# Performance work log

Measured on AMD Instinct MI355X. Metric: run time of the kernel, lower is better.

## Reference

```python
import jax, jax.numpy as jnp
import numpy as np

DIM = 2560
N_HEAD = 32
HEAD_DIM = 80
ROT_DIM = 32  # head_dim * partial_rotary_factor
INTER = 10240
EPS = 1e-5
BASE = 10000.0


def setup_inputs() -> dict:
    key = jax.random.key(0)
    ks = jax.random.split(key, 12)
    B, S, D, I = 1, 2048, DIM, INTER
    s = lambda k, shape, scale: (jax.random.normal(k, shape, jnp.float32) * scale)
    return {
        "x": s(ks[0], (B, S, D), 1.0),
        "input_pos": jnp.arange(S, dtype=jnp.int32),
        "mask": jnp.tril(jnp.ones((S, S), dtype=bool)),
        "ln_w": jnp.ones((D,), jnp.float32),
        "ln_b": jnp.zeros((D,), jnp.float32),
        "wqkv_w": s(ks[1], (3 * D, D), 0.02),
        "wqkv_b": jnp.zeros((3 * D,), jnp.float32),
        "wo_w": s(ks[2], (D, D), 0.02),
        "wo_b": jnp.zeros((D,), jnp.float32),
        "w1_w": s(ks[3], (I, D), 0.02),
        "w1_b": jnp.zeros((I,), jnp.float32),
        "w2_w": s(ks[4], (D, I), 0.02),
        "w2_b": jnp.zeros((D,), jnp.float32),
    }


def _rope_cos_sin(positions):
    # positions: [S] int; returns cos,sin of shape [S, ROT_DIM]
    inv_freq = 1.0 / (BASE ** (jnp.arange(0, ROT_DIM, 2, dtype=jnp.float32) / ROT_DIM))
    freqs = positions.astype(jnp.float32)[:, None] * inv_freq[None, :]  # [S, ROT/2]
    emb = jnp.concatenate([freqs, freqs], axis=-1)  # [S, ROT]
    return jnp.cos(emb), jnp.sin(emb)


def _rotate_half(t):
    t1, t2 = jnp.split(t, 2, axis=-1)
    return jnp.concatenate([-t2, t1], axis=-1)


def _apply_rope(t, cos, sin):
    # t: [B,H,S,hd]; rotary applied to first ROT_DIM dims (partial rotary)
    t_rot, t_pass = t[..., :ROT_DIM], t[..., ROT_DIM:]
    t_rot = t_rot * cos[None, None] + _rotate_half(t_rot) * sin[None, None]
    return jnp.concatenate([t_rot, t_pass], axis=-1)


def reference(x, input_pos, mask, ln_w, ln_b, wqkv_w, wqkv_b, wo_w, wo_b,
              w1_w, w1_b, w2_w, w2_b):
    B, S, D = x.shape
    H, hd = N_HEAD, HEAD_DIM
    # shared LayerNorm (parallel block)
    mu = jnp.mean(x, axis=-1, keepdims=True)
    var = jnp.mean(jnp.square(x - mu), axis=-1, keepdims=True)
    h = (x - mu) * jax.lax.rsqrt(var + EPS) * ln_w + ln_b

    # fused QKV
    qkv = h @ wqkv_w.T + wqkv_b  # [B,S,3D]
    q, k, v = jnp.split(qkv, 3, axis=-1)
    q = q.reshape(B, S, H, hd).transpose(0, 2, 1, 3)  # [B,H,S,hd]
    k = k.reshape(B, S, H, hd).transpose(0, 2, 1, 3)
    v = v.reshape(B, S, H, hd).transpose(0, 2, 1, 3)

    cos, sin = _rope_cos_sin(input_pos)
    q = _apply_rope(q, cos, sin)
    k = _apply_rope(k, cos, sin)

    # causal attention
    scores = jnp.einsum("bhqd,bhkd->bhqk", q, k) / np.sqrt(hd).astype(np.float32)
    scores = jnp.where(mask[None, None], scores, jnp.float32(-1e9))
    attn = jax.nn.softmax(scores, axis=-1)
    y = jnp.einsum("bhqk,bhkd->bhqd", attn, v)  # [B,H,S,hd]
    y = y.transpose(0, 2, 1, 3).reshape(B, S, D)
    attn_out = y @ wo_w.T + wo_b

    # fused MLP (phi2: gelu_new / tanh approx)
    ffn = jax.nn.gelu(h @ w1_w.T + w1_b, approximate=True) @ w2_w.T + w2_b

    return attn_out + ffn + x
```

## Files before the change

kernel.cpp:

```cpp
#include <hip/hip_runtime.h>
#include <cstdint>

#define S_LEN 2048
#define DMODEL 2560
#define NHEADS 32
#define HDIM 80
#define DINTER 10240

typedef unsigned short u16;
typedef __bf16 bf16x8 __attribute__((ext_vector_type(8)));
typedef float f32x4 __attribute__((ext_vector_type(4)));

__device__ __forceinline__ float us2f(u16 u) {
  return __builtin_bit_cast(float, ((uint32_t)u) << 16);
}
__device__ __forceinline__ u16 f2us(float f) {
  uint32_t x = __builtin_bit_cast(uint32_t, f);
  x += 0x7fffu + ((x >> 16) & 1u);
  return (u16)(x >> 16);
}

typedef __attribute__((address_space(1))) void gas_void;
typedef __attribute__((address_space(3))) void las_void;
__device__ __forceinline__ void gld16(const void* g, void* l) {
  __builtin_amdgcn_global_load_lds((gas_void*)g, (las_void*)l, 16, 0, 0);
}

#define VMW(N) asm volatile("s_waitcnt vmcnt(" #N ")" ::: "memory")
#define BARRIER()                          \
  do {                                     \
    asm volatile("" ::: "memory");         \
    __builtin_amdgcn_s_barrier();          \
    asm volatile("" ::: "memory");         \
  } while (0)

__global__ void f2b_kernel(const float* __restrict__ src, u16* __restrict__ dst) {
  const size_t i = ((size_t)blockIdx.x * 256 + threadIdx.x) * 8;
  const float4 a = *(const float4*)(src + i);
  const float4 b = *(const float4*)(src + i + 4);
  u16 o[8] = {f2us(a.x), f2us(a.y), f2us(a.z), f2us(a.w),
              f2us(b.x), f2us(b.y), f2us(b.z), f2us(b.w)};
  *(uint4*)(dst + i) = *(uint4*)o;
}

__global__ void initout_kernel(const float* __restrict__ x,
                               const float* __restrict__ wo_b,
                               const float* __restrict__ w2_b,
                               float* __restrict__ out) {
  const size_t idx = ((size_t)blockIdx.x * 256 + threadIdx.x) * 4;
  const int c0 = (int)(idx % DMODEL);
  const float4 vx = *(const float4*)(x + idx);
  const float4 b1 = *(const float4*)(wo_b + c0);
  const float4 b2 = *(const float4*)(w2_b + c0);
  float4 vo;
  vo.x = vx.x + b1.x + b2.x;
  vo.y = vx.y + b1.y + b2.y;
  vo.z = vx.z + b1.z + b2.z;
  vo.w = vx.w + b1.w + b2.w;
  *(float4*)(out + idx) = vo;
}

__global__ void ln_kernel(const float* __restrict__ x, const float* __restrict__ w,
                          const float* __restrict__ b, u16* __restrict__ h) {
  const int s = blockIdx.x, tid = threadIdx.x;
  const float* xr = x + (size_t)s * DMODEL;
  float v[10];
  float sum = 0.f, sq = 0.f;
#pragma unroll
  for (int j = 0; j < 10; j++) {
    v[j] = xr[tid + j * 256];
    sum += v[j];
    sq += v[j] * v[j];
  }
#pragma unroll
  for (int o = 32; o > 0; o >>= 1) {
    sum += __shfl_down(sum, o, 64);
    sq += __shfl_down(sq, o, 64);
  }
  __shared__ float red[8];
  const int wave = tid >> 6, lane = tid & 63;
  if (lane == 0) { red[wave] = sum; red[4 + wave] = sq; }
  __syncthreads();
  sum = red[0] + red[1] + red[2] + red[3];
  sq = red[4] + red[5] + red[6] + red[7];
  const float mu = sum * (1.0f / DMODEL);
  const float var = sq * (1.0f / DMODEL) - mu * mu;
  const float rstd = rsqrtf(var + 1e-5f);
  u16* hr = h + (size_t)s * DMODEL;
#pragma unroll
  for (int j = 0; j < 10; j++) {
    const int d = tid + j * 256;
    hr[d] = f2us((v[j] - mu) * rstd * w[d] + b[d]);
  }
}

template <int ACT, int MODE>
__launch_bounds__(512, 2)
__global__ void gemm256(const u16* __restrict__ A, const u16* __restrict__ B,
                        const float* __restrict__ bias, void* __restrict__ Cv,
                        int M, int N, int K) {
  __shared__ __align__(16) u16 lds[4][16384];
  const int tid = threadIdx.x;
  const int w = tid >> 6, lane = tid & 63;
  const int quad = lane >> 4, l15 = lane & 15;
  const int wm = w >> 2, wn = w & 3;

  const int nwg = gridDim.x * gridDim.y;
  const int flat = blockIdx.x + gridDim.x * blockIdx.y;
  const int swz = (flat & 7) * (nwg >> 3) + (flat >> 3);
  const int ntN = N >> 8;
  const int bm = swz / ntN, bn = swz % ntN;

  const int Kc = K / gridDim.z;
  const int k0 = Kc * blockIdx.z;
  const int nt = Kc >> 6;

  const int stgCol = (((lane & 7) ^ ((lane >> 3) & 7)) * 8);
  const u16* Ag = A + ((size_t)bm * 256 + w * 8 + (lane >> 3)) * K + k0 + stgCol;
  const u16* Bg = B + ((size_t)bn * 256 + w * 8 + (lane >> 3)) * K + k0 + stgCol;

  const int q8 = quad * 8;
  const int swz3 = (l15 & 7) * 8;
  const int arow = wm * 64 + l15;
  const int brow = wn * 32 + l15;

#define STG_HALF(MAT, GP, BUF, HF, KT)                                       \
  do {                                                                       \
    gld16((GP) + (size_t)((HF) * 128) * K + (size_t)(KT) * 64,               \
          &lds[(BUF) * 2 + (MAT)][(HF) * 8192 + w * 512]);                   \
    gld16((GP) + (size_t)((HF) * 128 + 64) * K + (size_t)(KT) * 64,          \
          &lds[(BUF) * 2 + (MAT)][(HF) * 8192 + 4096 + w * 512]);            \
  } while (0)

#define LDS_A(DST, BUF, MH)                                                  \
  _Pragma("unroll") for (int mf_ = 0; mf_ < 4; mf_++)                        \
  _Pragma("unroll") for (int kk_ = 0; kk_ < 2; kk_++)                        \
      DST[mf_][kk_] = *(const bf16x8*)&lds[(BUF) * 2]                        \
          [(arow + (MH) * 128 + mf_ * 16) * 64 + ((kk_ * 32 + q8) ^ swz3)];

#define LDS_B(DST, BUF, NH)                                                  \
  _Pragma("unroll") for (int nf_ = 0; nf_ < 2; nf_++)                        \
  _Pragma("unroll") for (int kk_ = 0; kk_ < 2; kk_++)                        \
      DST[nf_][kk_] = *(const bf16x8*)&lds[(BUF) * 2 + 1]                    \
          [(brow + (NH) * 128 + nf_ * 16) * 64 + ((kk_ * 32 + q8) ^ swz3)];

#define MFMA_C(MH, NH, AF, BF)                                               \
  do {                                                                       \
    __builtin_amdgcn_s_setprio(1);                                           \
    _Pragma("unroll") for (int kk_ = 0; kk_ < 2; kk_++)                      \
    _Pragma("unroll") for (int mf_ = 0; mf_ < 4; mf_++)                      \
    _Pragma("unroll") for (int nf_ = 0; nf_ < 2; nf_++)                      \
        acc[(MH) * 4 + mf_][(NH) * 2 + nf_] =                                \
            __builtin_amdgcn_mfma_f32_16x16x32_bf16(                         \
                AF[mf_][kk_], BF[nf_][kk_],                                  \
                acc[(MH) * 4 + mf_][(NH) * 2 + nf_], 0, 0, 0);               \
    __builtin_amdgcn_s_setprio(0);                                           \
  } while (0)

  f32x4 acc[8][4] = {};
  bf16x8 aH0[4][2], aH1[4][2], bH0[2][2], bH1[2][2];

  STG_HALF(0, Ag, 0, 0, 0);
  STG_HALF(1, Bg, 0, 0, 0);
  STG_HALF(1, Bg, 0, 1, 0);
  STG_HALF(0, Ag, 0, 1, 0);
  VMW(4);
  BARRIER();
  LDS_A(aH0, 0, 0);
  LDS_B(bH0, 0, 0);

  for (int t = 0; t < nt; ++t) {
    const int bc = t & 1, ob = bc ^ 1;
    const bool more = (t + 1 < nt);
    VMW(0);
    BARRIER();
    if (more) {
      STG_HALF(0, Ag, ob, 0, t + 1);
      STG_HALF(1, Bg, ob, 0, t + 1);
    }
    LDS_B(bH1, bc, 1);
    MFMA_C(0, 0, aH0, bH0);
    if (more) STG_HALF(1, Bg, ob, 1, t + 1);
    LDS_A(aH1, bc, 1);
    MFMA_C(0, 1, aH0, bH1);
    if (more) STG_HALF(0, Ag, ob, 1, t + 1);
    MFMA_C(1, 1, aH1, bH1);
    VMW(4);
    BARRIER();
    MFMA_C(1, 0, aH1, bH0);
    if (more) {
      LDS_A(aH0, ob, 0);
      LDS_B(bH0, ob, 0);
    }
  }

#pragma unroll
  for (int nh = 0; nh < 2; nh++)
#pragma unroll
    for (int nf = 0; nf < 2; nf++) {
      const int col = bn * 256 + nh * 128 + wn * 32 + nf * 16 + l15;
      const float bv = (MODE == 0) ? bias[col] : 0.f;
#pragma unroll
      for (int mh = 0; mh < 2; mh++)
#pragma unroll
        for (int mf = 0; mf < 4; mf++) {
          const int row0 = bm * 256 + mh * 128 + wm * 64 + mf * 16 + quad * 4;
#pragma unroll
          for (int r = 0; r < 4; r++) {
            float v = acc[mh * 4 + mf][nh * 2 + nf][r] + bv;
            if (ACT == 1) {
              const float tt = v * (0.7978845608f + 0.0356774081f * v * v);
              v = 0.5f * v * (1.0f + tanhf(tt));
            }
            if (MODE == 0)
              ((u16*)Cv)[(size_t)(row0 + r) * N + col] = f2us(v);
            else
              atomicAdd((float*)Cv + (size_t)(row0 + r) * N + col, v);
          }
        }
    }
#undef STG_HALF
#undef LDS_A
#undef LDS_B
#undef MFMA_C
}

__global__ void rope_kernel(u16* __restrict__ qkv, const int* __restrict__ pos) {
  const int idx = blockIdx.x * 256 + threadIdx.x;
  const int i = idx & 15;
  const int which = (idx >> 4) & 1;
  const int hh = (idx >> 5) & 31;
  const int s = idx >> 10;
  const float p = (float)pos[s];
  const float freq = p * expf(-0.57564627324851f * (float)i);
  float sn, c;
  sincosf(freq, &sn, &c);
  u16* base = qkv + (size_t)s * (3 * DMODEL) + which * DMODEL + hh * HDIM + i;
  const float t0 = us2f(base[0]), t1 = us2f(base[16]);
  base[0] = f2us(t0 * c - t1 * sn);
  base[16] = f2us(t1 * c + t0 * sn);
}

__global__ void attn_kernel(const u16* __restrict__ qkv, u16* __restrict__ y) {
  const int qt = (int)gridDim.x - 1 - (int)blockIdx.x;
  const int h = blockIdx.y;
  const int tid = threadIdx.x, wave = tid >> 6, lane = tid & 63;
  const int quad = lane >> 4, l15 = lane & 15;
  const int qbase = qt * 64;

  __shared__ __align__(16) u16 Qs[64 * 104];
  __shared__ __align__(16) u16 Ks[2][64 * 104];
  __shared__ __align__(16) u16 Vts[2][80 * 88];
  __shared__ __align__(16) u16 Ps[4][2][16 * 40];

  if (tid < 128) {
    const int b = tid >> 6, r = tid & 63;
    u16* z = &Ks[b][r * 104 + 80];
    *(uint4*)z = uint4{0, 0, 0, 0};
    *(uint4*)(z + 8) = uint4{0, 0, 0, 0};
  } else if (tid < 192) {
    const int r = tid & 63;
    u16* z = &Qs[r * 104 + 80];
    *(uint4*)z = uint4{0, 0, 0, 0};
    *(uint4*)(z + 8) = uint4{0, 0, 0, 0};
    *(uint4*)(z + 16) = uint4{0, 0, 0, 0};
  }

  {
    const int r = tid >> 2, c = tid & 3;
    const u16* src = qkv + (size_t)(qbase + r) * (3 * DMODEL) + h * HDIM + c * 20;
    u16* dst = Qs + r * 104 + c * 20;
#pragma unroll
    for (int j = 0; j < 5; j++) {
      ushort4 uv = *(const ushort4*)(src + j * 4);
      ushort4 ov;
      ov.x = f2us(us2f(uv.x) * 0.11180339887f);
      ov.y = f2us(us2f(uv.y) * 0.11180339887f);
      ov.z = f2us(us2f(uv.z) * 0.11180339887f);
      ov.w = f2us(us2f(uv.w) * 0.11180339887f);
      *(ushort4*)(dst + j * 4) = ov;
    }
  }

  {
    const int r = tid >> 2, c4 = (tid & 3) * 20;
    const u16* sK = qkv + (size_t)r * (3 * DMODEL) + DMODEL + h * HDIM + c4;
    u16* dK = &Ks[0][r * 104 + c4];
#pragma unroll
    for (int j = 0; j < 5; j++) *(uint2*)(dK + j * 4) = *(const uint2*)(sK + j * 4);
  }
  if (tid < 160) {
    const int p = tid & 31, cc = tid >> 5;
    const u16* sV = qkv + (size_t)(2 * p) * (3 * DMODEL) + 2 * DMODEL + h * HDIM + cc * 16;
    const uint4 a0 = *(const uint4*)sV;
    const uint4 b0 = *(const uint4*)(sV + 8);
    const uint4 a1 = *(const uint4*)(sV + 3 * DMODEL);
    const uint4 b1 = *(const uint4*)(sV + 3 * DMODEL + 8);
    const uint32_t A0[8] = {a0.x, a0.y, a0.z, a0.w, b0.x, b0.y, b0.z, b0.w};
    const uint32_t A1[8] = {a1.x, a1.y, a1.z, a1.w, b1.x, b1.y, b1.z, b1.w};
    uint32_t* dV = (uint32_t*)Vts[0];
#pragma unroll
    for (int d = 0; d < 16; d++) {
      const int j = d >> 1, s = (d & 1) * 16;
      const uint32_t o = ((A0[j] >> s) & 0xffffu) | (((A1[j] >> s) & 0xffffu) << 16);
      dV[(cc * 16 + d) * 44 + p] = o;
    }
  }

  float m_i[4], l_i[4];
  f32x4 oacc[5] = {};
#pragma unroll
  for (int r = 0; r < 4; r++) { m_i[r] = -1e30f; l_i[r] = 0.f; }

  __syncthreads();

  bf16x8 aq[3];
#pragma unroll
  for (int ks = 0; ks < 3; ks++)
    aq[ks] = *(const bf16x8*)&Qs[(wave * 16 + l15) * 104 + ks * 32 + quad * 8];

  const int n_iter = qt + 1;
  uint2 kr[5];
  uint4 v0a = {}, v0b = {}, v1a = {}, v1b = {};

  for (int it = 0; it < n_iter; ++it) {
    const int cur = it & 1;
    const bool more = (it + 1 < n_iter);
    if (more) {
      const int kcn = (it + 1) * 64;
      const int r = tid >> 2, c4 = (tid & 3) * 20;
      const u16* sK = qkv + (size_t)(kcn + r) * (3 * DMODEL) + DMODEL + h * HDIM + c4;
#pragma unroll
      for (int j = 0; j < 5; j++) kr[j] = *(const uint2*)(sK + j * 4);
      if (tid < 160) {
        const int p = tid & 31, cc = tid >> 5;
        const u16* sV =
            qkv + (size_t)(kcn + 2 * p) * (3 * DMODEL) + 2 * DMODEL + h * HDIM + cc * 16;
        v0a = *(const uint4*)sV;
        v0b = *(const uint4*)(sV + 8);
        v1a = *(const uint4*)(sV + 3 * DMODEL);
        v1b = *(const uint4*)(sV + 3 * DMODEL + 8);
      }
    }

    const int kc0 = it * 64;
    f32x4 st[4] = {};
#pragma unroll
    for (int ks = 0; ks < 3; ks++)
#pragma unroll
      for (int t = 0; t < 4; t++) {
        bf16x8 bk = *(const bf16x8*)&Ks[cur][(t * 16 + l15) * 104 + ks * 32 + quad * 8];
        st[t] = __builtin_amdgcn_mfma_f32_16x16x32_bf16(aq[ks], bk, st[t], 0, 0, 0);
      }

    float sv[4][4], mx[4];
    if (it == qt) {
#pragma unroll
      for (int r = 0; r < 4; r++) {
        const int qr = qbase + wave * 16 + quad * 4 + r;
#pragma unroll
        for (int t = 0; t < 4; t++) {
          const int kc = kc0 + t * 16 + l15;
          sv[t][r] = (kc <= qr) ? st[t][r] : -1e30f;
        }
      }
    } else {
#pragma unroll
      for (int r = 0; r < 4; r++)
#pragma unroll
        for (int t = 0; t < 4; t++) sv[t][r] = st[t][r];
    }
#pragma unroll
    for (int r = 0; r < 4; r++)
      mx[r] = fmaxf(fmaxf(sv[0][r], sv[1][r]), fmaxf(sv[2][r], sv[3][r]));
#pragma unroll
    for (int o = 1; o < 16; o <<= 1)
#pragma unroll
      for (int r = 0; r < 4; r++) mx[r] = fmaxf(mx[r], __shfl_xor(mx[r], o, 64));

    float alpha[4], rs[4];
#pragma unroll
    for (int r = 0; r < 4; r++) {
      const float mnew = fmaxf(m_i[r], mx[r]);
      alpha[r] = __expf(m_i[r] - mnew);
      m_i[r] = mnew;
      const float p0 = __expf(sv[0][r] - mnew);
      const float p1 = __expf(sv[1][r] - mnew);
      const float p2 = __expf(sv[2][r] - mnew);
      const float p3 = __expf(sv[3][r] - mnew);
      rs[r] = (p0 + p1) + (p2 + p3);
      const int ro = (quad * 4 + r) * 40;
      Ps[wave][0][ro + l15] = f2us(p0);
      Ps[wave][0][ro + 16 + l15] = f2us(p1);
      Ps[wave][1][ro + l15] = f2us(p2);
      Ps[wave][1][ro + 16 + l15] = f2us(p3);
    }
#pragma unroll
    for (int o = 1; o < 16; o <<= 1)
#pragma unroll
      for (int r = 0; r < 4; r++) rs[r] += __shfl_xor(rs[r], o, 64);
#pragma unroll
    for (int r = 0; r < 4; r++) l_i[r] = l_i[r] * alpha[r] + rs[r];
#pragma unroll
    for (int dt = 0; dt < 5; dt++)
#pragma unroll
      for (int r = 0; r < 4; r++) oacc[dt][r] *= alpha[r];

    bf16x8 pf0 = *(const bf16x8*)&Ps[wave][0][l15 * 40 + quad * 8];
    bf16x8 pf1 = *(const bf16x8*)&Ps[wave][1][l15 * 40 + quad * 8];
#pragma unroll
    for (int dt = 0; dt < 5; dt++) {
      bf16x8 vf0 = *(const bf16x8*)&Vts[cur][(dt * 16 + l15) * 88 + quad * 8];
      bf16x8 vf1 = *(const bf16x8*)&Vts[cur][(dt * 16 + l15) * 88 + 32 + quad * 8];
      oacc[dt] = __builtin_amdgcn_mfma_f32_16x16x32_bf16(pf0, vf0, oacc[dt], 0, 0, 0);
      oacc[dt] = __builtin_amdgcn_mfma_f32_16x16x32_bf16(pf1, vf1, oacc[dt], 0, 0, 0);
    }

    if (more) {
      const int r = tid >> 2, c4 = (tid & 3) * 20;
      u16* dK = &Ks[cur ^ 1][r * 104 + c4];
#pragma unroll
      for (int j = 0; j < 5; j++) *(uint2*)(dK + j * 4) = kr[j];
      if (tid < 160) {
        const int p = tid & 31, cc = tid >> 5;
        const uint32_t A0[8] = {v0a.x, v0a.y, v0a.z, v0a.w,
                                v0b.x, v0b.y, v0b.z, v0b.w};
        const uint32_t A1[8] = {v1a.x, v1a.y, v1a.z, v1a.w,
                                v1b.x, v1b.y, v1b.z, v1b.w};
        uint32_t* dV = (uint32_t*)Vts[cur ^ 1];
#pragma unroll
        for (int d = 0; d < 16; d++) {
          const int j = d >> 1, s = (d & 1) * 16;
          const uint32_t o =
              ((A0[j] >> s) & 0xffffu) | (((A1[j] >> s) & 0xffffu) << 16);
          dV[(cc * 16 + d) * 44 + p] = o;
        }
      }
    }
    __syncthreads();
  }

#pragma unroll
  for (int dt = 0; dt < 5; dt++)
#pragma unroll
    for (int r = 0; r < 4; r++) {
      const int row = qbase + wave * 16 + quad * 4 + r;
      y[(size_t)row * DMODEL + h * HDIM + dt * 16 + l15] = f2us(oacc[dt][r] / l_i[r]);
    }
}

extern "C" void kernel_launch(void* const* d_in, const int* in_sizes, int n_in,
                              void* d_out, int out_size, void* d_ws, size_t ws_size,
                              hipStream_t stream) {
  const float* x = (const float*)d_in[0];
  const int* pos = (const int*)d_in[1];
  const float* ln_w = (const float*)d_in[3];
  const float* ln_b = (const float*)d_in[4];
  const float* wqkv_w = (const float*)d_in[5];
  const float* wqkv_b = (const float*)d_in[6];
  const float* wo_w = (const float*)d_in[7];
  const float* wo_b = (const float*)d_in[8];
  const float* w1_w = (const float*)d_in[9];
  const float* w1_b = (const float*)d_in[10];
  const float* w2_w = (const float*)d_in[11];
  const float* w2_b = (const float*)d_in[12];
  float* out = (float*)d_out;

  char* ws = (char*)d_ws;
  u16* wbuf = (u16*)(ws);
  u16* h = (u16*)(ws + 52428800);
  u16* ffn1 = (u16*)(ws + 62914560);
  u16* qkv = (u16*)(ws + 62914560);
  u16* yAtt = (u16*)(ws + 94371840);

  ln_kernel<<<S_LEN, 256, 0, stream>>>(x, ln_w, ln_b, h);
  initout_kernel<<<(S_LEN * DMODEL / 4) / 256, 256, 0, stream>>>(x, wo_b, w2_b, out);

  f2b_kernel<<<(DINTER * DMODEL) / 2048, 256, 0, stream>>>(w1_w, wbuf);
  gemm256<1, 0><<<dim3(DINTER / 256, S_LEN / 256, 1), 512, 0, stream>>>(
      h, wbuf, w1_b, ffn1, S_LEN, DINTER, DMODEL);
  f2b_kernel<<<(DMODEL * DINTER) / 2048, 256, 0, stream>>>(w2_w, wbuf);
  gemm256<0, 2><<<dim3(DMODEL / 256, S_LEN / 256, 5), 512, 0, stream>>>(
      ffn1, wbuf, w2_b, out, S_LEN, DMODEL, DINTER);

  f2b_kernel<<<(3 * DMODEL * DMODEL) / 2048, 256, 0, stream>>>(wqkv_w, wbuf);
  gemm256<0, 0><<<dim3(3 * DMODEL / 256, S_LEN / 256, 1), 512, 0, stream>>>(
      h, wbuf, wqkv_b, qkv, S_LEN, 3 * DMODEL, DMODEL);
  rope_kernel<<<(S_LEN * NHEADS * 2 * 16) / 256, 256, 0, stream>>>(qkv, pos);
  attn_kernel<<<dim3(S_LEN / 64, NHEADS), 256, 0, stream>>>(qkv, yAtt);
  f2b_kernel<<<(DMODEL * DMODEL) / 2048, 256, 0, stream>>>(wo_w, wbuf);
  gemm256<0, 2><<<dim3(DMODEL / 256, S_LEN / 256, 2), 512, 0, stream>>>(
      yAtt, wbuf, wo_b, out, S_LEN, DMODEL, DMODEL);
}
```

Baseline: 959.6 us.

## Restructure GEMM mainloop to triple-buffered K=32 tiles with single-phase MFMA body

The 256x256 GEMM now steps through K in 32-wide tiles instead of 64, using a three-stage LDS ring (3x32KB) in place of the double-buffered interleaved half-tile schedule. Loads run two tiles ahead, with one barrier per tile. Each wave now owns a contiguous 128x64 output block, and the LDS swizzle is changed to match the 32-element rows. The aim is a simpler loop with deeper prefetch and less LDS. The cost is twice as many barriers per K, and the fine-grained interleaving of LDS reads with MFMAs is lost.

New measurement: 1.036 ms. +8.0%, slower.

```diff
diff --git a/kernel.cpp b/kernel.cpp
--- a/kernel.cpp
+++ b/kernel.cpp
@@ -99,7 +99,7 @@
 __global__ void gemm256(const u16* __restrict__ A, const u16* __restrict__ B,
                         const float* __restrict__ bias, void* __restrict__ Cv,
                         int M, int N, int K) {
-  __shared__ __align__(16) u16 lds[4][16384];
+  __shared__ __align__(16) u16 lds[3][16384];
   const int tid = threadIdx.x;
   const int w = tid >> 6, lane = tid & 63;
   const int quad = lane >> 4, l15 = lane & 15;
@@ -113,116 +113,84 @@
 
   const int Kc = K / gridDim.z;
   const int k0 = Kc * blockIdx.z;
-  const int nt = Kc >> 6;
-
-  const int stgCol = (((lane & 7) ^ ((lane >> 3) & 7)) * 8);
-  const u16* Ag = A + ((size_t)bm * 256 + w * 8 + (lane >> 3)) * K + k0 + stgCol;
-  const u16* Bg = B + ((size_t)bn * 256 + w * 8 + (lane >> 3)) * K + k0 + stgCol;
-
-  const int q8 = quad * 8;
-  const int swz3 = (l15 & 7) * 8;
-  const int arow = wm * 64 + l15;
-  const int brow = wn * 32 + l15;
-
-#define STG_HALF(MAT, GP, BUF, HF, KT)                                       \
+  const int nt = Kc >> 5;
+
+  const int g = ((lane & 3) ^ ((lane >> 3) & 3)) * 8;
+  const u16* Ag = A + ((size_t)bm * 256 + w * 32 + (lane >> 2)) * K + k0 + g;
+  const u16* Bg = B + ((size_t)bn * 256 + w * 32 + (lane >> 2)) * K + k0 + g;
+  const size_t k16 = (size_t)16 * K;
+  const int aw = w * 1024;
+
+  const int rswz = (quad ^ ((l15 >> 1) & 3)) * 8;
+  const int arow = wm * 128 + l15;
+  const int brow = wn * 64 + l15;
+
+#define STG(T)                                                               \
   do {                                                                       \
-    gld16((GP) + (size_t)((HF) * 128) * K + (size_t)(KT) * 64,               \
-          &lds[(BUF) * 2 + (MAT)][(HF) * 8192 + w * 512]);                   \
-    gld16((GP) + (size_t)((HF) * 128 + 64) * K + (size_t)(KT) * 64,          \
-          &lds[(BUF) * 2 + (MAT)][(HF) * 8192 + 4096 + w * 512]);            \
+    const int q_ = (T) % 3;                                                  \
+    const size_t ko_ = (size_t)(T) * 32;                                     \
+    gld16(Ag + ko_, &lds[q_][aw]);                                           \
+    gld16(Ag + ko_ + k16, &lds[q_][aw + 512]);                               \
+    gld16(Bg + ko_, &lds[q_][8192 + aw]);                                    \
+    gld16(Bg + ko_ + k16, &lds[q_][8192 + aw + 512]);                        \
   } while (0)
 
-#define LDS_A(DST, BUF, MH)                                                  \
-  _Pragma("unroll") for (int mf_ = 0; mf_ < 4; mf_++)                        \
-  _Pragma("unroll") for (int kk_ = 0; kk_ < 2; kk_++)                        \
-      DST[mf_][kk_] = *(const bf16x8*)&lds[(BUF) * 2]                        \
-          [(arow + (MH) * 128 + mf_ * 16) * 64 + ((kk_ * 32 + q8) ^ swz3)];
-
-#define LDS_B(DST, BUF, NH)                                                  \
-  _Pragma("unroll") for (int nf_ = 0; nf_ < 2; nf_++)                        \
-  _Pragma("unroll") for (int kk_ = 0; kk_ < 2; kk_++)                        \
-      DST[nf_][kk_] = *(const bf16x8*)&lds[(BUF) * 2 + 1]                    \
-          [(brow + (NH) * 128 + nf_ * 16) * 64 + ((kk_ * 32 + q8) ^ swz3)];
-
-#define MFMA_C(MH, NH, AF, BF)                                               \
+#define TILE_BODY(T)                                                         \
   do {                                                                       \
+    const int qb_ = (T) % 3;                                                 \
+    bf16x8 aF[8], bF[4];                                                     \
+    _Pragma("unroll") for (int mf_ = 0; mf_ < 8; mf_++)                      \
+        aF[mf_] = *(const bf16x8*)&lds[qb_][(arow + mf_ * 16) * 32 + rswz];  \
+    _Pragma("unroll") for (int nf_ = 0; nf_ < 4; nf_++)                      \
+        bF[nf_] = *(const bf16x8*)&lds[qb_][8192 + (brow + nf_ * 16) * 32 + rswz]; \
     __builtin_amdgcn_s_setprio(1);                                           \
-    _Pragma("unroll") for (int kk_ = 0; kk_ < 2; kk_++)                      \
-    _Pragma("unroll") for (int mf_ = 0; mf_ < 4; mf_++)                      \
-    _Pragma("unroll") for (int nf_ = 0; nf_ < 2; nf_++)                      \
-        acc[(MH) * 4 + mf_][(NH) * 2 + nf_] =                                \
-            __builtin_amdgcn_mfma_f32_16x16x32_bf16(                         \
-                AF[mf_][kk_], BF[nf_][kk_],                                  \
-                acc[(MH) * 4 + mf_][(NH) * 2 + nf_], 0, 0, 0);               \
+    _Pragma("unroll") for (int mf_ = 0; mf_ < 8; mf_++)                      \
+    _Pragma("unroll") for (int nf_ = 0; nf_ < 4; nf_++)                      \
+        acc[mf_][nf_] = __builtin_amdgcn_mfma_f32_16x16x32_bf16(             \
+            aF[mf_], bF[nf_], acc[mf_][nf_], 0, 0, 0);                       \
     __builtin_amdgcn_s_setprio(0);                                           \
   } while (0)
 
   f32x4 acc[8][4] = {};
-  bf16x8 aH0[4][2], aH1[4][2], bH0[2][2], bH1[2][2];
-
-  STG_HALF(0, Ag, 0, 0, 0);
-  STG_HALF(1, Bg, 0, 0, 0);
-  STG_HALF(1, Bg, 0, 1, 0);
-  STG_HALF(0, Ag, 0, 1, 0);
-  VMW(4);
-  BARRIER();
-  LDS_A(aH0, 0, 0);
-  LDS_B(bH0, 0, 0);
-
-  for (int t = 0; t < nt; ++t) {
-    const int bc = t & 1, ob = bc ^ 1;
-    const bool more = (t + 1 < nt);
+
+  STG(0);
+  STG(1);
+
+  for (int t = 0; t < nt - 1; ++t) {
+    VMW(4);
+    BARRIER();
+    if (t + 2 < nt) STG(t + 2);
+    TILE_BODY(t);
+  }
+  {
     VMW(0);
     BARRIER();
-    if (more) {
-      STG_HALF(0, Ag, ob, 0, t + 1);
-      STG_HALF(1, Bg, ob, 0, t + 1);
-    }
-    LDS_B(bH1, bc, 1);
-    MFMA_C(0, 0, aH0, bH0);
-    if (more) STG_HALF(1, Bg, ob, 1, t + 1);
-    LDS_A(aH1, bc, 1);
-    MFMA_C(0, 1, aH0, bH1);
-    if (more) STG_HALF(0, Ag, ob, 1, t + 1);
-    MFMA_C(1, 1, aH1, bH1);
-    VMW(4);
-    BARRIER();
-    MFMA_C(1, 0, aH1, bH0);
-    if (more) {
-      LDS_A(aH0, ob, 0);
-      LDS_B(bH0, ob, 0);
-    }
-  }
-
-#pragma unroll
-  for (int nh = 0; nh < 2; nh++)
-#pragma unroll
-    for (int nf = 0; nf < 2; nf++) {
-      const int col = bn * 256 + nh * 128 + wn * 32 + nf * 16 + l15;
-      const float bv = (MODE == 0) ? bias[col] : 0.f;
-#pragma unroll
-      for (int mh = 0; mh < 2; mh++)
-#pragma unroll
-        for (int mf = 0; mf < 4; mf++) {
-          const int row0 = bm * 256 + mh * 128 + wm * 64 + mf * 16 + quad * 4;
-#pragma unroll
-          for (int r = 0; r < 4; r++) {
-            float v = acc[mh * 4 + mf][nh * 2 + nf][r] + bv;
-            if (ACT == 1) {
-              const float tt = v * (0.7978845608f + 0.0356774081f * v * v);
-              v = 0.5f * v * (1.0f + tanhf(tt));
-            }
-            if (MODE == 0)
-              ((u16*)Cv)[(size_t)(row0 + r) * N + col] = f2us(v);
-            else
-              atomicAdd((float*)Cv + (size_t)(row0 + r) * N + col, v);
-          }
+    TILE_BODY(nt - 1);
+  }
+
+#pragma unroll
+  for (int nf = 0; nf < 4; nf++) {
+    const int col = bn * 256 + wn * 64 + nf * 16 + l15;
+    const float bv = (MODE == 0) ? bias[col] : 0.f;
+#pragma unroll
+    for (int mf = 0; mf < 8; mf++) {
+      const int row0 = bm * 256 + wm * 128 + mf * 16 + quad * 4;
+#pragma unroll
+      for (int r = 0; r < 4; r++) {
+        float v = acc[mf][nf][r] + bv;
+        if (ACT == 1) {
+          const float tt = v * (0.7978845608f + 0.0356774081f * v * v);
+          v = 0.5f * v * (1.0f + tanhf(tt));
         }
-    }
-#undef STG_HALF
-#undef LDS_A
-#undef LDS_B
-#undef MFMA_C
+        if (MODE == 0)
+          ((u16*)Cv)[(size_t)(row0 + r) * N + col] = f2us(v);
+        else
+          atomicAdd((float*)Cv + (size_t)(row0 + r) * N + col, v);
+      }
+    }
+  }
+#undef STG
+#undef TILE_BODY
 }
 
 __global__ void rope_kernel(u16* __restrict__ qkv, const int* __restrict__ pos) {
```
